# Kernel optimization log

Hardware: AMD Instinct MI355X
Metric: run time of the kernel (lower is better)

## Reference

```python
import jax, jax.numpy as jnp
import numpy as np

HEADS = 8
DIM_HEAD = 64
ROPE_BASE = 10000.0


def _rope_rotate(t):
    """lucidrains-style interleaved RoPE on t: [B, H, N, D]."""
    n, d = t.shape[-2], t.shape[-1]
    inv_freq = 1.0 / (ROPE_BASE ** (jnp.arange(0, d, 2, dtype=jnp.float32) / d))  # [D/2]
    freqs = jnp.arange(n, dtype=jnp.float32)[:, None] * inv_freq[None, :]          # [N, D/2]
    freqs = jnp.repeat(freqs, 2, axis=-1)                                           # [N, D], interleaved
    cos = jnp.cos(freqs).astype(t.dtype)
    sin = jnp.sin(freqs).astype(t.dtype)
    # rotate_half with interleaved pairs: (x1, x2) -> (-x2, x1)
    t2 = t.reshape(t.shape[:-1] + (d // 2, 2))
    rot = jnp.stack([-t2[..., 1], t2[..., 0]], axis=-1).reshape(t.shape)
    return t * cos + rot * sin


def setup_inputs() -> dict:
    key = jax.random.key(0)
    k1, k2, k3, k4 = jax.random.split(key, 4)
    B, N, DIM = 8, 1024, 512
    hidden = HEADS * DIM_HEAD  # 512
    x = jax.random.normal(k1, (B, N, DIM), dtype=jnp.float32)
    pos_bias = jax.random.normal(k2, (HEADS, N, N), dtype=jnp.float32) * 0.1
    w_qkv = jax.random.normal(k3, (DIM, hidden * 3), dtype=jnp.float32) * (DIM ** -0.5)
    w_out = jax.random.normal(k4, (hidden, DIM), dtype=jnp.float32) * (hidden ** -0.5)
    return {"x": x, "pos_bias": pos_bias, "w_qkv": w_qkv, "w_out": w_out}


def reference(x, pos_bias, w_qkv, w_out):
    B, N, _ = x.shape
    qkv = x @ w_qkv                                   # [B, N, 3*H*D]
    q, k, v = jnp.split(qkv, 3, axis=-1)

    def split_heads(t):
        return t.reshape(B, N, HEADS, DIM_HEAD).transpose(0, 2, 1, 3)  # [B, H, N, D]

    q, k, v = map(split_heads, (q, k, v))
    q = q * (DIM_HEAD ** -0.5)
    q = _rope_rotate(q)
    k = _rope_rotate(k)
    sim = jnp.einsum('bhid,bhjd->bhij', q, k) + pos_bias  # pos_bias [H,N,N] broadcasts over B
    attn = jax.nn.softmax(sim, axis=-1)                    # max-subtracted softmax (stable)
    out = jnp.einsum('bhij,bhjd->bhid', attn, v)
    out = out.transpose(0, 2, 1, 3).reshape(B, N, HEADS * DIM_HEAD)
    return out @ w_out
```

## Files before the change

### kernel.cpp

```cpp
#include <hip/hip_runtime.h>

#define DEV __device__ __forceinline__

typedef __attribute__((ext_vector_type(8))) short bf16x8;
typedef __attribute__((ext_vector_type(4))) short bf16x4;
typedef __attribute__((ext_vector_type(4))) float f32x4;
typedef __attribute__((ext_vector_type(4))) unsigned int u32x4;

constexpr int Bb = 8;
constexpr int Nn = 1024;
constexpr int DIMm = 512;
constexpr int Hh = 8;
constexpr int Dh = 64;
constexpr int Mm = Bb * Nn;
constexpr float LN10K = 9.210340371976184f;

DEV short f2bf(float f) {
  unsigned int u = __float_as_uint(f);
  u += 0x7fffu + ((u >> 16) & 1u);
  return (short)(u >> 16);
}

DEV bf16x8 comb(bf16x4 lo, bf16x4 hi) {
  bf16x8 r;
  r[0] = lo[0]; r[1] = lo[1]; r[2] = lo[2]; r[3] = lo[3];
  r[4] = hi[0]; r[5] = hi[1]; r[6] = hi[2]; r[7] = hi[3];
  return r;
}

DEV f32x4 mfma16(bf16x8 a, bf16x8 b, f32x4 c) {
  return __builtin_amdgcn_mfma_f32_16x16x32_bf16(a, b, c, 0, 0, 0);
}

__global__ void prep_kernel(const float* __restrict__ x, const float* __restrict__ wq,
                            const float* __restrict__ wo, short* __restrict__ x_bf,
                            short* __restrict__ wqkvT, short* __restrict__ woutT) {
  int stride = gridDim.x * blockDim.x;
  int t = blockIdx.x * blockDim.x + threadIdx.x;
  for (int i = t; i < Mm * DIMm / 4; i += stride) {
    float4 v = ((const float4*)x)[i];
    bf16x4 o;
    o[0] = f2bf(v.x); o[1] = f2bf(v.y); o[2] = f2bf(v.z); o[3] = f2bf(v.w);
    *(bf16x4*)(x_bf + (size_t)i * 4) = o;
  }
  for (int i = t; i < 1536 * 512; i += stride) {
    int n = i >> 9, k = i & 511;
    wqkvT[i] = f2bf(wq[(size_t)k * 1536 + n]);
  }
  for (int i = t; i < 512 * 512; i += stride) {
    int n = i >> 9, k = i & 511;
    woutT[i] = f2bf(wo[(size_t)k * 512 + n]);
  }
}

template <int QKV>
__global__ __launch_bounds__(256) void gemm_k(const short* __restrict__ A,
                                              const short* __restrict__ Bt,
                                              float* __restrict__ outF,
                                              short* __restrict__ qr,
                                              short* __restrict__ kr,
                                              short* __restrict__ vt) {
  __shared__ short Al[128][40];
  __shared__ short Bl[128][40];
  const int tid = threadIdx.x;
  const int lane = tid & 63;
  const int wid = tid >> 6;
  const int wm = wid >> 1, wn = wid & 1;
  const int li = lane & 15, g4 = (lane >> 4) << 2;
  const int m0 = blockIdx.x * 128, n0 = blockIdx.y * 128;

  f32x4 zero4 = {0.f, 0.f, 0.f, 0.f};
  f32x4 acc[4][4];
#pragma unroll
  for (int i = 0; i < 4; ++i)
#pragma unroll
    for (int j = 0; j < 4; ++j) acc[i][j] = zero4;

  for (int kt = 0; kt < 512; kt += 32) {
#pragma unroll
    for (int p = 0; p < 2; ++p) {
      int e = (tid + p * 256) * 8;
      int r = e >> 5, c = e & 31;
      *(u32x4*)(&Al[r][c]) = *(const u32x4*)(A + (size_t)(m0 + r) * 512 + kt + c);
      *(u32x4*)(&Bl[r][c]) = *(const u32x4*)(Bt + (size_t)(n0 + r) * 512 + kt + c);
    }
    __syncthreads();
    bf16x8 af[4], bfr[4];
#pragma unroll
    for (int mt = 0; mt < 4; ++mt) {
      int row = wm * 64 + mt * 16 + li;
      af[mt] = comb(*(const bf16x4*)(&Al[row][g4]), *(const bf16x4*)(&Al[row][16 + g4]));
    }
#pragma unroll
    for (int nt = 0; nt < 4; ++nt) {
      int row = wn * 64 + nt * 16 + li;
      bfr[nt] = comb(*(const bf16x4*)(&Bl[row][g4]), *(const bf16x4*)(&Bl[row][16 + g4]));
    }
#pragma unroll
    for (int mt = 0; mt < 4; ++mt)
#pragma unroll
      for (int nt = 0; nt < 4; ++nt)
        acc[mt][nt] = mfma16(af[mt], bfr[nt], acc[mt][nt]);
    __syncthreads();
  }

  if (QKV == 0) {
#pragma unroll
    for (int mt = 0; mt < 4; ++mt) {
      int mb = m0 + wm * 64 + mt * 16 + g4;
#pragma unroll
      for (int nt = 0; nt < 4; ++nt) {
        int c = n0 + wn * 64 + nt * 16 + li;
#pragma unroll
        for (int r = 0; r < 4; ++r) outF[(size_t)(mb + r) * 512 + c] = acc[mt][nt][r];
      }
    }
  } else {
    const int sec = n0 >> 9;
#pragma unroll
    for (int mt = 0; mt < 4; ++mt) {
      int mb = m0 + wm * 64 + mt * 16 + g4;
      int b_ = mb >> 10;
      int nb = mb & 1023;
#pragma unroll
      for (int nt = 0; nt < 4; ++nt) {
        int c = n0 + wn * 64 + nt * 16 + li;
        int cs = c & 511;
        int hh = cs >> 6, d = cs & 63;
        if (sec == 2) {
          bf16x4 pk;
#pragma unroll
          for (int r = 0; r < 4; ++r) pk[r] = f2bf(acc[mt][nt][r]);
          *(bf16x4*)(vt + ((size_t)(b_ * Hh + hh) * Dh + d) * Nn + nb) = pk;
        } else {
          float invf = __expf(-(float)(d & ~1) * (LN10K / 64.f));
          short* dst = (sec == 0 ? qr : kr) + ((size_t)(b_ * Hh + hh) * Nn + nb) * Dh + d;
#pragma unroll
          for (int r = 0; r < 4; ++r) {
            float v0 = acc[mt][nt][r];
            float vp = __shfl_xor(v0, 1, 64);
            float fr = (float)(nb + r) * invf;
            float sn, cs2;
            __sincosf(fr, &sn, &cs2);
            float rot = (d & 1) ? vp : -vp;
            float res = v0 * cs2 + rot * sn;
            if (sec == 0) res *= 0.125f;
            dst[(size_t)r * Dh] = f2bf(res);
          }
        }
      }
    }
  }
}

__global__ __launch_bounds__(256) void attn_k(const short* __restrict__ qr,
                                              const short* __restrict__ kr,
                                              const short* __restrict__ vt,
                                              const float* __restrict__ bias,
                                              short* __restrict__ ao) {
  __shared__ short Kl[64][72];
  __shared__ short Vl[64][72];
  const int tid = threadIdx.x, lane = tid & 63, w = tid >> 6;
  const int li = lane & 15, g4 = (lane >> 4) << 2;
  const int bh = blockIdx.y, h = bh & 7, b_ = bh >> 3;
  const int i0 = blockIdx.x * 64;
  const int iq = i0 + w * 16 + li;

  const short* qrow = qr + ((size_t)bh * Nn + iq) * Dh;
  bf16x8 qf[2];
#pragma unroll
  for (int kk = 0; kk < 2; ++kk)
    qf[kk] = comb(*(const bf16x4*)(qrow + kk * 32 + g4),
                  *(const bf16x4*)(qrow + kk * 32 + 16 + g4));

  const short* Kb = kr + (size_t)bh * Nn * Dh;
  const short* Vb = vt + (size_t)bh * Dh * Nn;
  const float* brow = bias + ((size_t)h * Nn + iq) * Nn;

  float m_run = -1e30f, l_run = 0.f;
  f32x4 zero4 = {0.f, 0.f, 0.f, 0.f};
  f32x4 acc[4];
#pragma unroll
  for (int i = 0; i < 4; ++i) acc[i] = zero4;

  for (int j0 = 0; j0 < Nn; j0 += 64) {
#pragma unroll
    for (int pp = 0; pp < 2; ++pp) {
      int e = (tid + pp * 256) * 8;
      int r = e >> 6, c = e & 63;
      *(u32x4*)(&Kl[r][c]) = *(const u32x4*)(Kb + (size_t)(j0 + r) * Dh + c);
      *(u32x4*)(&Vl[r][c]) = *(const u32x4*)(Vb + (size_t)r * Nn + j0 + c);
    }
    __syncthreads();

    f32x4 s[4];
#pragma unroll
    for (int js = 0; js < 4; ++js) {
      f32x4 sa = zero4;
#pragma unroll
      for (int kk = 0; kk < 2; ++kk) {
        bf16x8 kf = comb(*(const bf16x4*)(&Kl[js * 16 + li][kk * 32 + g4]),
                         *(const bf16x4*)(&Kl[js * 16 + li][kk * 32 + 16 + g4]));
        sa = mfma16(kf, qf[kk], sa);
      }
      f32x4 bb = *(const f32x4*)(brow + j0 + js * 16 + g4);
      s[js] = sa + bb;
    }
    float mx = -1e30f;
#pragma unroll
    for (int js = 0; js < 4; ++js)
#pragma unroll
      for (int r = 0; r < 4; ++r) mx = fmaxf(mx, s[js][r]);
    mx = fmaxf(mx, __shfl_xor(mx, 16, 64));
    mx = fmaxf(mx, __shfl_xor(mx, 32, 64));
    float m_new = fmaxf(m_run, mx);
    float scale = __expf(m_run - m_new);
    float rs = 0.f;
#pragma unroll
    for (int js = 0; js < 4; ++js)
#pragma unroll
      for (int r = 0; r < 4; ++r) {
        float p = __expf(s[js][r] - m_new);
        s[js][r] = p;
        rs += p;
      }
    rs += __shfl_xor(rs, 16, 64);
    rs += __shfl_xor(rs, 32, 64);
    l_run = l_run * scale + rs;
    m_run = m_new;
    float fs[4];
#pragma unroll
    for (int r = 0; r < 4; ++r) fs[r] = __shfl(scale, g4 + r, 64);
#pragma unroll
    for (int dt = 0; dt < 4; ++dt)
#pragma unroll
      for (int r = 0; r < 4; ++r) acc[dt][r] *= fs[r];
    bf16x8 pf[2];
#pragma unroll
    for (int kk = 0; kk < 2; ++kk) {
      bf16x8 t;
#pragma unroll
      for (int r = 0; r < 4; ++r) {
        t[r] = f2bf(s[2 * kk][r]);
        t[4 + r] = f2bf(s[2 * kk + 1][r]);
      }
      pf[kk] = t;
    }
#pragma unroll
    for (int dt = 0; dt < 4; ++dt) {
#pragma unroll
      for (int kk = 0; kk < 2; ++kk) {
        bf16x8 vf = comb(*(const bf16x4*)(&Vl[dt * 16 + li][kk * 32 + g4]),
                         *(const bf16x4*)(&Vl[dt * 16 + li][kk * 32 + 16 + g4]));
        acc[dt] = mfma16(pf[kk], vf, acc[dt]);
      }
    }
    __syncthreads();
  }
  float rl = 1.f / l_run;
  float fr[4];
#pragma unroll
  for (int r = 0; r < 4; ++r) fr[r] = __shfl(rl, g4 + r, 64);
#pragma unroll
  for (int dt = 0; dt < 4; ++dt)
#pragma unroll
    for (int r = 0; r < 4; ++r) {
      int i_ = i0 + w * 16 + g4 + r;
      ao[((size_t)(b_ * Nn + i_)) * 512 + h * 64 + dt * 16 + li] = f2bf(acc[dt][r] * fr[r]);
    }
}

extern "C" void kernel_launch(void* const* d_in, const int* in_sizes, int n_in,
                              void* d_out, int out_size, void* d_ws, size_t ws_size,
                              hipStream_t stream) {
  const float* x = (const float*)d_in[0];
  const float* pb = (const float*)d_in[1];
  const float* wq = (const float*)d_in[2];
  const float* wo = (const float*)d_in[3];
  float* out = (float*)d_out;

  short* w = (short*)d_ws;
  short* x_bf = w;  w += (size_t)Mm * DIMm;
  short* wqkvT = w; w += 1536 * 512;
  short* woutT = w; w += 512 * 512;
  short* qr = w;    w += (size_t)Mm * DIMm;
  short* kr = w;    w += (size_t)Mm * DIMm;
  short* vt = w;    w += (size_t)Mm * DIMm;
  short* ao = x_bf;

  prep_kernel<<<1024, 256, 0, stream>>>(x, wq, wo, x_bf, wqkvT, woutT);
  gemm_k<1><<<dim3(64, 12), 256, 0, stream>>>(x_bf, wqkvT, nullptr, qr, kr, vt);
  attn_k<<<dim3(16, 64), 256, 0, stream>>>(qr, kr, vt, pb, ao);
  gemm_k<0><<<dim3(64, 4), 256, 0, stream>>>(ao, woutT, out, nullptr, nullptr, nullptr);
}
```

Measured before the change: 117.3 us.

## Overhaul attention loop: direct-to-LDS loads, swizzled tiles, exp2 softmax with lazy rescale

The attention kernel now handles 128 keys per iteration. K/V tiles are loaded straight into XOR-swizzled LDS with global_load_lds, and the bias is prefetched into registers before the barrier. Softmax works in base 2, with log2e folded into q and the bias, and the running-max rescale is skipped while the max grows by no more than 8. Blocks are reordered so heads of the same batch run adjacently, and P is packed with v_cvt_pk_bf16. The QKV epilogue reads RoPE cos/sin from a precomputed table instead of calling sincos. The kernel now has only one barrier between the LDS reads and the next overwrite, which carries some race risk, and the lazy rescale may cost a little accuracy.

```diff
diff --git a/kernel.cpp b/kernel.cpp
--- a/kernel.cpp
+++ b/kernel.cpp
@@ -14,11 +14,18 @@
 constexpr int Dh = 64;
 constexpr int Mm = Bb * Nn;
 constexpr float LN10K = 9.210340371976184f;
+constexpr float LOG2E = 1.4426950408889634f;
 
 DEV short f2bf(float f) {
   unsigned int u = __float_as_uint(f);
   u += 0x7fffu + ((u >> 16) & 1u);
   return (short)(u >> 16);
+}
+
+DEV unsigned int cvtpk(float lo, float hi) {
+  unsigned int r;
+  asm("v_cvt_pk_bf16_f32 %0, %1, %2" : "=v"(r) : "v"(lo), "v"(hi));
+  return r;
 }
 
 DEV bf16x8 comb(bf16x4 lo, bf16x4 hi) {
@@ -32,9 +39,16 @@
   return __builtin_amdgcn_mfma_f32_16x16x32_bf16(a, b, c, 0, 0, 0);
 }
 
+DEV void gload16(const void* g, void* l) {
+  __builtin_amdgcn_global_load_lds(
+      (const __attribute__((address_space(1))) void*)g,
+      (__attribute__((address_space(3))) void*)l, 16, 0, 0);
+}
+
 __global__ void prep_kernel(const float* __restrict__ x, const float* __restrict__ wq,
                             const float* __restrict__ wo, short* __restrict__ x_bf,
-                            short* __restrict__ wqkvT, short* __restrict__ woutT) {
+                            short* __restrict__ wqkvT, short* __restrict__ woutT,
+                            float2* __restrict__ tab) {
   int stride = gridDim.x * blockDim.x;
   int t = blockIdx.x * blockDim.x + threadIdx.x;
   for (int i = t; i < Mm * DIMm / 4; i += stride) {
@@ -51,6 +65,13 @@
     int n = i >> 9, k = i & 511;
     woutT[i] = f2bf(wo[(size_t)k * 512 + n]);
   }
+  for (int i = t; i < Nn * 32; i += stride) {
+    int n = i >> 5, d2 = i & 31;
+    float fr = (float)n * __expf(-(float)(2 * d2) * (LN10K / 64.f));
+    float sn, cs;
+    __sincosf(fr, &sn, &cs);
+    tab[i] = make_float2(cs, sn);
+  }
 }
 
 template <int QKV>
@@ -59,7 +80,8 @@
                                               float* __restrict__ outF,
                                               short* __restrict__ qr,
                                               short* __restrict__ kr,
-                                              short* __restrict__ vt) {
+                                              short* __restrict__ vt,
+                                              const float2* __restrict__ tab) {
   __shared__ short Al[128][40];
   __shared__ short Bl[128][40];
   const int tid = threadIdx.x;
@@ -128,23 +150,20 @@
         int cs = c & 511;
         int hh = cs >> 6, d = cs & 63;
         if (sec == 2) {
-          bf16x4 pk;
-#pragma unroll
-          for (int r = 0; r < 4; ++r) pk[r] = f2bf(acc[mt][nt][r]);
-          *(bf16x4*)(vt + ((size_t)(b_ * Hh + hh) * Dh + d) * Nn + nb) = pk;
+          uint2 st;
+          st.x = cvtpk(acc[mt][nt][0], acc[mt][nt][1]);
+          st.y = cvtpk(acc[mt][nt][2], acc[mt][nt][3]);
+          *(uint2*)(vt + ((size_t)(b_ * Hh + hh) * Dh + d) * Nn + nb) = st;
         } else {
-          float invf = __expf(-(float)(d & ~1) * (LN10K / 64.f));
           short* dst = (sec == 0 ? qr : kr) + ((size_t)(b_ * Hh + hh) * Nn + nb) * Dh + d;
 #pragma unroll
           for (int r = 0; r < 4; ++r) {
             float v0 = acc[mt][nt][r];
             float vp = __shfl_xor(v0, 1, 64);
-            float fr = (float)(nb + r) * invf;
-            float sn, cs2;
-            __sincosf(fr, &sn, &cs2);
+            float2 cssn = tab[(size_t)(nb + r) * 32 + (d >> 1)];
             float rot = (d & 1) ? vp : -vp;
-            float res = v0 * cs2 + rot * sn;
-            if (sec == 0) res *= 0.125f;
+            float res = v0 * cssn.x + rot * cssn.y;
+            if (sec == 0) res *= 0.125f * LOG2E;
             dst[(size_t)r * Dh] = f2bf(res);
           }
         }
@@ -153,17 +172,21 @@
   }
 }
 
-__global__ __launch_bounds__(256) void attn_k(const short* __restrict__ qr,
-                                              const short* __restrict__ kr,
-                                              const short* __restrict__ vt,
-                                              const float* __restrict__ bias,
-                                              short* __restrict__ ao) {
-  __shared__ short Kl[64][72];
-  __shared__ short Vl[64][72];
+__global__ __launch_bounds__(256, 4) void attn_k(const short* __restrict__ qr,
+                                                 const short* __restrict__ kr,
+                                                 const short* __restrict__ vt,
+                                                 const float* __restrict__ bias,
+                                                 short* __restrict__ ao) {
+  __shared__ short Kl[128 * 64];
+  __shared__ short Vl[64 * 128];
   const int tid = threadIdx.x, lane = tid & 63, w = tid >> 6;
   const int li = lane & 15, g4 = (lane >> 4) << 2;
-  const int bh = blockIdx.y, h = bh & 7, b_ = bh >> 3;
-  const int i0 = blockIdx.x * 64;
+  const int bid = blockIdx.x;
+  const int h = bid & 7;
+  const int inner = bid >> 3;
+  const int b_ = inner >> 4, it = inner & 15;
+  const int bh = b_ * 8 + h;
+  const int i0 = it * 64;
   const int iq = i0 + w * 16 + li;
 
   const short* qrow = qr + ((size_t)bh * Nn + iq) * Dh;
@@ -173,8 +196,8 @@
     qf[kk] = comb(*(const bf16x4*)(qrow + kk * 32 + g4),
                   *(const bf16x4*)(qrow + kk * 32 + 16 + g4));
 
-  const short* Kb = kr + (size_t)bh * Nn * Dh;
-  const short* Vb = vt + (size_t)bh * Dh * Nn;
+  const char* KbB = (const char*)(kr + (size_t)bh * Nn * Dh);
+  const char* VbB = (const char*)(vt + (size_t)bh * Dh * Nn);
   const float* brow = bias + ((size_t)h * Nn + iq) * Nn;
 
   float m_run = -1e30f, l_run = 0.f;
@@ -183,91 +206,116 @@
 #pragma unroll
   for (int i = 0; i < 4; ++i) acc[i] = zero4;
 
-  for (int j0 = 0; j0 < Nn; j0 += 64) {
-#pragma unroll
-    for (int pp = 0; pp < 2; ++pp) {
-      int e = (tid + pp * 256) * 8;
-      int r = e >> 6, c = e & 63;
-      *(u32x4*)(&Kl[r][c]) = *(const u32x4*)(Kb + (size_t)(j0 + r) * Dh + c);
-      *(u32x4*)(&Vl[r][c]) = *(const u32x4*)(Vb + (size_t)r * Nn + j0 + c);
-    }
+  for (int j0 = 0; j0 < Nn; j0 += 128) {
+    f32x4 bb[8];
+#pragma unroll
+    for (int js = 0; js < 8; ++js)
+      bb[js] = *(const f32x4*)(brow + j0 + js * 16 + g4);
+
     __syncthreads();
-
-    f32x4 s[4];
-#pragma unroll
-    for (int js = 0; js < 4; ++js) {
-      f32x4 sa = zero4;
-#pragma unroll
-      for (int kk = 0; kk < 2; ++kk) {
-        bf16x8 kf = comb(*(const bf16x4*)(&Kl[js * 16 + li][kk * 32 + g4]),
-                         *(const bf16x4*)(&Kl[js * 16 + li][kk * 32 + 16 + g4]));
-        sa = mfma16(kf, qf[kk], sa);
-      }
-      f32x4 bb = *(const f32x4*)(brow + j0 + js * 16 + g4);
-      s[js] = sa + bb;
-    }
-    float mx = -1e30f;
-#pragma unroll
-    for (int js = 0; js < 4; ++js)
-#pragma unroll
-      for (int r = 0; r < 4; ++r) mx = fmaxf(mx, s[js][r]);
+#pragma unroll
+    for (int p = 0; p < 4; ++p) {
+      int L = (tid + p * 256) * 16;
+      int row = L >> 7, sb = L & 127;
+      int gb = sb ^ ((row & 7) << 4);
+      gload16(KbB + (size_t)(j0 + row) * 128 + gb, (char*)Kl + L);
+      int rv = L >> 8, sv = L & 255;
+      int gv = sv ^ ((rv & 7) << 4);
+      gload16(VbB + (size_t)rv * 2048 + (size_t)j0 * 2 + gv, (char*)Vl + L);
+    }
+    __syncthreads();
+
+    f32x4 s[8];
+#pragma unroll
+    for (int js = 0; js < 8; ++js) {
+      int row = js * 16 + li;
+      int sw = (row & 7) << 3;
+      const short* kb = Kl + row * 64;
+      f32x4 sa = bb[js] * LOG2E;
+      bf16x8 kf0 = comb(*(const bf16x4*)(kb + ((g4) ^ sw)),
+                        *(const bf16x4*)(kb + ((16 + g4) ^ sw)));
+      bf16x8 kf1 = comb(*(const bf16x4*)(kb + ((32 + g4) ^ sw)),
+                        *(const bf16x4*)(kb + ((48 + g4) ^ sw)));
+      sa = mfma16(kf0, qf[0], sa);
+      sa = mfma16(kf1, qf[1], sa);
+      s[js] = sa;
+    }
+
+    float mx = -3e38f;
+#pragma unroll
+    for (int js = 0; js < 8; ++js) {
+      float a = fmaxf(fmaxf(s[js][0], s[js][1]), fmaxf(s[js][2], s[js][3]));
+      mx = fmaxf(mx, a);
+    }
     mx = fmaxf(mx, __shfl_xor(mx, 16, 64));
     mx = fmaxf(mx, __shfl_xor(mx, 32, 64));
-    float m_new = fmaxf(m_run, mx);
-    float scale = __expf(m_run - m_new);
+
+    if (!__all(mx - m_run <= 8.0f)) {
+      float mn = fmaxf(m_run, mx);
+      float sc = __builtin_amdgcn_exp2f(m_run - mn);
+      l_run *= sc;
+      m_run = mn;
+      float fs0 = __shfl(sc, g4 + 0, 64), fs1 = __shfl(sc, g4 + 1, 64);
+      float fs2 = __shfl(sc, g4 + 2, 64), fs3 = __shfl(sc, g4 + 3, 64);
+#pragma unroll
+      for (int dt = 0; dt < 4; ++dt) {
+        acc[dt][0] *= fs0; acc[dt][1] *= fs1;
+        acc[dt][2] *= fs2; acc[dt][3] *= fs3;
+      }
+    }
+
     float rs = 0.f;
 #pragma unroll
-    for (int js = 0; js < 4; ++js)
+    for (int js = 0; js < 8; ++js)
 #pragma unroll
       for (int r = 0; r < 4; ++r) {
-        float p = __expf(s[js][r] - m_new);
+        float p = __builtin_amdgcn_exp2f(s[js][r] - m_run);
         s[js][r] = p;
         rs += p;
       }
     rs += __shfl_xor(rs, 16, 64);
     rs += __shfl_xor(rs, 32, 64);
-    l_run = l_run * scale + rs;
-    m_run = m_new;
-    float fs[4];
-#pragma unroll
-    for (int r = 0; r < 4; ++r) fs[r] = __shfl(scale, g4 + r, 64);
-#pragma unroll
-    for (int dt = 0; dt < 4; ++dt)
-#pragma unroll
-      for (int r = 0; r < 4; ++r) acc[dt][r] *= fs[r];
-    bf16x8 pf[2];
-#pragma unroll
-    for (int kk = 0; kk < 2; ++kk) {
-      bf16x8 t;
-#pragma unroll
-      for (int r = 0; r < 4; ++r) {
-        t[r] = f2bf(s[2 * kk][r]);
-        t[4 + r] = f2bf(s[2 * kk + 1][r]);
-      }
-      pf[kk] = t;
-    }
+    l_run += rs;
+
+    bf16x8 pf[4];
+#pragma unroll
+    for (int kk = 0; kk < 4; ++kk) {
+      union { bf16x8 v; unsigned int d[4]; } u;
+      u.d[0] = cvtpk(s[2 * kk][0], s[2 * kk][1]);
+      u.d[1] = cvtpk(s[2 * kk][2], s[2 * kk][3]);
+      u.d[2] = cvtpk(s[2 * kk + 1][0], s[2 * kk + 1][1]);
+      u.d[3] = cvtpk(s[2 * kk + 1][2], s[2 * kk + 1][3]);
+      pf[kk] = u.v;
+    }
+
 #pragma unroll
     for (int dt = 0; dt < 4; ++dt) {
-#pragma unroll
-      for (int kk = 0; kk < 2; ++kk) {
-        bf16x8 vf = comb(*(const bf16x4*)(&Vl[dt * 16 + li][kk * 32 + g4]),
-                         *(const bf16x4*)(&Vl[dt * 16 + li][kk * 32 + 16 + g4]));
+      int row = dt * 16 + li;
+      int sw = (row & 7) << 3;
+      const short* vb = Vl + row * 128;
+#pragma unroll
+      for (int kk = 0; kk < 4; ++kk) {
+        int c = kk * 32 + g4;
+        bf16x8 vf = comb(*(const bf16x4*)(vb + (c ^ sw)),
+                         *(const bf16x4*)(vb + ((c + 16) ^ sw)));
         acc[dt] = mfma16(pf[kk], vf, acc[dt]);
       }
     }
-    __syncthreads();
-  }
+  }
+
   float rl = 1.f / l_run;
-  float fr[4];
-#pragma unroll
-  for (int r = 0; r < 4; ++r) fr[r] = __shfl(rl, g4 + r, 64);
-#pragma unroll
-  for (int dt = 0; dt < 4; ++dt)
+  float fr0 = __shfl(rl, g4 + 0, 64), fr1 = __shfl(rl, g4 + 1, 64);
+  float fr2 = __shfl(rl, g4 + 2, 64), fr3 = __shfl(rl, g4 + 3, 64);
+#pragma unroll
+  for (int dt = 0; dt < 4; ++dt) {
+    float fr[4] = {fr0, fr1, fr2, fr3};
 #pragma unroll
     for (int r = 0; r < 4; ++r) {
       int i_ = i0 + w * 16 + g4 + r;
-      ao[((size_t)(b_ * Nn + i_)) * 512 + h * 64 + dt * 16 + li] = f2bf(acc[dt][r] * fr[r]);
-    }
+      ao[((size_t)(b_ * Nn + i_)) * 512 + h * 64 + dt * 16 + li] =
+          f2bf(acc[dt][r] * fr[r]);
+    }
+  }
 }
 
 extern "C" void kernel_launch(void* const* d_in, const int* in_sizes, int n_in,
@@ -286,10 +334,11 @@
   short* qr = w;    w += (size_t)Mm * DIMm;
   short* kr = w;    w += (size_t)Mm * DIMm;
   short* vt = w;    w += (size_t)Mm * DIMm;
+  float2* tab = (float2*)w; w += Nn * 32 * 4;
   short* ao = x_bf;
 
-  prep_kernel<<<1024, 256, 0, stream>>>(x, wq, wo, x_bf, wqkvT, woutT);
-  gemm_k<1><<<dim3(64, 12), 256, 0, stream>>>(x_bf, wqkvT, nullptr, qr, kr, vt);
-  attn_k<<<dim3(16, 64), 256, 0, stream>>>(qr, kr, vt, pb, ao);
-  gemm_k<0><<<dim3(64, 4), 256, 0, stream>>>(ao, woutT, out, nullptr, nullptr, nullptr);
-}
+  prep_kernel<<<1024, 256, 0, stream>>>(x, wq, wo, x_bf, wqkvT, woutT, tab);
+  gemm_k<1><<<dim3(64, 12), 256, 0, stream>>>(x_bf, wqkvT, nullptr, qr, kr, vt, tab);
+  attn_k<<<1024, 256, 0, stream>>>(qr, kr, vt, pb, ao);
+  gemm_k<0><<<dim3(64, 4), 256, 0, stream>>>(ao, woutT, out, nullptr, nullptr, nullptr, tab);
+}
```

New measurement: 122.4 us. 4.4% more time.
